# Kernel optimization log

Measured on AMD Instinct MI355X. Metric: run time of the kernel, lower is better.

## Reference

```python
import jax, jax.numpy as jnp
import numpy as np

N_NODES = 100000
N_EDGES = 1600000
HID = 32


def gcn_conv(x, W, b, src, dst, num_nodes):
    # PyG GCNConv: h = X W; out = D^{-1/2}(A+I)D^{-1/2} h + b
    # (self loops already appended to src/dst by caller)
    h = x @ W
    deg = jax.ops.segment_sum(jnp.ones_like(dst, dtype=h.dtype), dst,
                              num_segments=num_nodes)
    dinv = jnp.where(deg > 0, jax.lax.rsqrt(deg), 0.0)
    norm = dinv[src] * dinv[dst]                      # [E+N]
    msg = h[src] * norm[:, None]                      # gather + scale
    out = jax.ops.segment_sum(msg, dst, num_segments=num_nodes)  # scatter-add
    return out + b


def setup_inputs() -> dict:
    key = jax.random.key(0)
    ks = jax.random.split(key, 12)
    x = jax.random.normal(ks[0], (N_NODES, 2), dtype=jnp.float32)
    edge_index = jax.random.randint(ks[1], (2, N_EDGES), 0, N_NODES,
                                    dtype=jnp.int32)
    s = 0.2  # small init scale
    return {
        "x": x,
        "edge_index": edge_index,
        "fc1_W": jax.random.normal(ks[2], (2, HID), jnp.float32) * s,
        "fc1_b": jnp.zeros((HID,), jnp.float32),
        "c1_W": jax.random.normal(ks[3], (HID, HID), jnp.float32) * s,
        "c1_b": jnp.zeros((HID,), jnp.float32),
        "c2_W": jax.random.normal(ks[4], (HID, HID), jnp.float32) * s,
        "c2_b": jnp.zeros((HID,), jnp.float32),
        "c3_W": jax.random.normal(ks[5], (HID, HID), jnp.float32) * s,
        "c3_b": jnp.zeros((HID,), jnp.float32),
        "fc2_W": jax.random.normal(ks[6], (HID, HID), jnp.float32) * s,
        "fc2_b": jnp.zeros((HID,), jnp.float32),
        "fc3_W": jax.random.normal(ks[7], (HID, 1), jnp.float32) * s,
        "fc3_b": jnp.zeros((1,), jnp.float32),
    }


def reference(x, edge_index, fc1_W, fc1_b, c1_W, c1_b, c2_W, c2_b,
              c3_W, c3_b, fc2_W, fc2_b, fc3_W, fc3_b):
    num_nodes = x.shape[0]
    loop = jnp.arange(num_nodes, dtype=edge_index.dtype)
    src = jnp.concatenate([edge_index[0], loop])  # add self loops
    dst = jnp.concatenate([edge_index[1], loop])
    h = jax.nn.relu(x @ fc1_W + fc1_b)
    h = jax.nn.relu(gcn_conv(h, c1_W, c1_b, src, dst, num_nodes))
    h = jax.nn.relu(gcn_conv(h, c2_W, c2_b, src, dst, num_nodes))
    h = jax.nn.relu(gcn_conv(h, c3_W, c3_b, src, dst, num_nodes))
    h = jax.nn.relu(h @ fc2_W + fc2_b)
    return h @ fc3_W + fc3_b
```

## Files before the change

kernel.cpp:

```cpp
#include <hip/hip_runtime.h>
#include <hip/hip_fp16.h>

#define NN 100000
#define NE 1600000
#define HID 32
#define NBK 391
#define CAP 4608
#define CHUNK 8192

__device__ __forceinline__ float4 load_h4(const __half* p) {
    uint2 u = *(const uint2*)p;
    __half2 h0 = *(__half2*)&u.x;
    __half2 h1 = *(__half2*)&u.y;
    float2 a = __half22float2(h0);
    float2 b = __half22float2(h1);
    return make_float4(a.x, a.y, b.x, b.y);
}

__global__ __launch_bounds__(256) void partA_kernel(
        const int* __restrict__ src, const int* __restrict__ dst,
        int* __restrict__ bktcur, int* __restrict__ bedges) {
    __shared__ int cache[CHUNK];
    __shared__ int hist[NBK];
    __shared__ int lofs[NBK];
    int t = threadIdx.x;
    int base = blockIdx.x * CHUNK;
    for (int i = t; i < NBK; i += 256) hist[i] = 0;
    __syncthreads();
    for (int i = t; i < CHUNK; i += 256) {
        int e = base + i;
        if (e < NE) {
            int d = dst[e];
            cache[i] = d;
            atomicAdd(&hist[d >> 8], 1);
        }
    }
    __syncthreads();
    for (int i = t; i < NBK; i += 256)
        lofs[i] = hist[i] ? atomicAdd(&bktcur[i], hist[i]) : 0;
    __syncthreads();
    for (int i = t; i < CHUNK; i += 256) {
        int e = base + i;
        if (e < NE) {
            int d = cache[i];
            int s = src[e];
            int b = d >> 8;
            int rel = atomicAdd(&lofs[b], 1);
            if (rel < CAP) bedges[b * CAP + rel] = (s << 8) | (d & 255);
        }
    }
}

__global__ __launch_bounds__(256) void bucket_csr_kernel(
        const int* __restrict__ bedges, const int* __restrict__ bktcur,
        const float* __restrict__ x, float* __restrict__ dinv,
        int* __restrict__ srcidx, int* __restrict__ rbeg, int* __restrict__ rend,
        float4* __restrict__ xpack) {
    __shared__ int ldeg[256];
    __shared__ int lcur[256];
    __shared__ int wsum[256];
    int b = blockIdx.x, t = threadIdx.x;
    int ebeg = b * CAP;
    int cnt = min(bktcur[b], CAP);
    int n0 = b << 8;
    ldeg[t] = 0;
    __syncthreads();
    for (int e = t; e < cnt; e += 256)
        atomicAdd(&ldeg[bedges[ebeg + e] & 255], 1);
    __syncthreads();
    int a = ldeg[t];
    wsum[t] = a;
    __syncthreads();
    for (int off = 1; off < 256; off <<= 1) {
        int xv = (t >= off) ? wsum[t - off] : 0;
        __syncthreads();
        wsum[t] += xv;
        __syncthreads();
    }
    int excl = wsum[t] - a;
    lcur[t] = excl;
    int n = n0 + t;
    if (n < NN) {
        float dv = rsqrtf((float)(a + 1));
        rbeg[n] = ebeg + excl;
        rend[n] = ebeg + excl + a;
        dinv[n] = dv;
        float2 xv2 = *(const float2*)&x[2 * n];
        xpack[n] = make_float4(xv2.x, xv2.y, dv, 0.f);
    }
    __syncthreads();
    for (int e = t; e < cnt; e += 256) {
        int w = bedges[ebeg + e];
        int pos = atomicAdd(&lcur[w & 255], 1);
        srcidx[ebeg + pos] = (unsigned)w >> 8;
    }
}

__global__ __launch_bounds__(256) void conv1_kernel(
        const float4* __restrict__ xpack, const int* __restrict__ rbeg,
        const int* __restrict__ rend, const int* __restrict__ srcidx,
        const float* __restrict__ dinv, const float* __restrict__ W1,
        const float* __restrict__ b1, const float* __restrict__ W,
        const float* __restrict__ bias, __half* __restrict__ hs_out) {
    __shared__ float wl[HID * HID];
    __shared__ float agg[8][HID];
    int tid = threadIdx.x;
    int base8 = blockIdx.x * 8;
#pragma unroll
    for (int i = 0; i < 4; ++i) wl[tid + 256 * i] = W[tid + 256 * i];
    int wave = tid >> 6, lane = tid & 63;
    int g = lane >> 3;
    int l = lane & 7;
    float4 w0q = *(const float4*)&W1[l << 2];
    float4 w1q = *(const float4*)&W1[HID + (l << 2)];
    float4 bq  = *(const float4*)&b1[l << 2];
#pragma unroll
    for (int rep = 0; rep < 2; ++rep) {
        int ln = wave * 2 + rep;
        int n = base8 + ln;
        int beg = rbeg[n], end = rend[n];
        float4 acc0 = make_float4(0.f, 0.f, 0.f, 0.f);
        float4 acc1 = make_float4(0.f, 0.f, 0.f, 0.f);
        int e = beg + g;
        for (; e + 8 < end; e += 16) {
            float4 p0 = xpack[srcidx[e]];
            float4 p1 = xpack[srcidx[e + 8]];
            acc0.x += fmaxf(p0.x * w0q.x + p0.y * w1q.x + bq.x, 0.f) * p0.z;
            acc0.y += fmaxf(p0.x * w0q.y + p0.y * w1q.y + bq.y, 0.f) * p0.z;
            acc0.z += fmaxf(p0.x * w0q.z + p0.y * w1q.z + bq.z, 0.f) * p0.z;
            acc0.w += fmaxf(p0.x * w0q.w + p0.y * w1q.w + bq.w, 0.f) * p0.z;
            acc1.x += fmaxf(p1.x * w0q.x + p1.y * w1q.x + bq.x, 0.f) * p1.z;
            acc1.y += fmaxf(p1.x * w0q.y + p1.y * w1q.y + bq.y, 0.f) * p1.z;
            acc1.z += fmaxf(p1.x * w0q.z + p1.y * w1q.z + bq.z, 0.f) * p1.z;
            acc1.w += fmaxf(p1.x * w0q.w + p1.y * w1q.w + bq.w, 0.f) * p1.z;
        }
        if (e < end) {
            float4 p0 = xpack[srcidx[e]];
            acc0.x += fmaxf(p0.x * w0q.x + p0.y * w1q.x + bq.x, 0.f) * p0.z;
            acc0.y += fmaxf(p0.x * w0q.y + p0.y * w1q.y + bq.y, 0.f) * p0.z;
            acc0.z += fmaxf(p0.x * w0q.z + p0.y * w1q.z + bq.z, 0.f) * p0.z;
            acc0.w += fmaxf(p0.x * w0q.w + p0.y * w1q.w + bq.w, 0.f) * p0.z;
        }
        acc0.x += acc1.x; acc0.y += acc1.y; acc0.z += acc1.z; acc0.w += acc1.w;
#pragma unroll
        for (int m = 8; m < 64; m <<= 1) {
            acc0.x += __shfl_xor(acc0.x, m);
            acc0.y += __shfl_xor(acc0.y, m);
            acc0.z += __shfl_xor(acc0.z, m);
            acc0.w += __shfl_xor(acc0.w, m);
        }
        if (g == 0) {
            float4 ps = xpack[n];
            float dv = ps.z;
            float4 r;
            r.x = (acc0.x + fmaxf(ps.x * w0q.x + ps.y * w1q.x + bq.x, 0.f) * dv) * dv;
            r.y = (acc0.y + fmaxf(ps.x * w0q.y + ps.y * w1q.y + bq.y, 0.f) * dv) * dv;
            r.z = (acc0.z + fmaxf(ps.x * w0q.z + ps.y * w1q.z + bq.z, 0.f) * dv) * dv;
            r.w = (acc0.w + fmaxf(ps.x * w0q.w + ps.y * w1q.w + bq.w, 0.f) * dv) * dv;
            *(float4*)&agg[ln][l << 2] = r;
        }
    }
    __syncthreads();
    int ln = tid >> 5, j = tid & 31;
    int n = base8 + ln;
    float v = 0.f;
#pragma unroll
    for (int k = 0; k < HID; ++k) v += agg[ln][k] * wl[k * HID + j];
    v = fmaxf(v + bias[j], 0.f) * dinv[n];
    hs_out[(n << 5) + j] = __float2half(v);
}

template <bool OUTSCALE, bool FUSE23>
__global__ __launch_bounds__(256) void conv_fused_kernel(
        const __half* __restrict__ hs_in, const int* __restrict__ rbeg,
        const int* __restrict__ rend, const int* __restrict__ srcidx,
        const float* __restrict__ dinv, const float* __restrict__ W,
        const float* __restrict__ bias, const float* __restrict__ W2,
        const float* __restrict__ b2, const float* __restrict__ W3,
        const float* __restrict__ b3, void* __restrict__ hs_out_v) {
    __shared__ float wl[HID * HID];
    __shared__ float wl2[FUSE23 ? HID * HID : 1];
    __shared__ float agg[8][HID];
    int tid = threadIdx.x;
    int base8 = blockIdx.x * 8;
#pragma unroll
    for (int i = 0; i < 4; ++i) wl[tid + 256 * i] = W[tid + 256 * i];
    if (FUSE23) {
#pragma unroll
        for (int i = 0; i < 4; ++i) wl2[tid + 256 * i] = W2[tid + 256 * i];
    }
    int wave = tid >> 6, lane = tid & 63;
    int g = lane >> 3;
    int l = lane & 7;
#pragma unroll
    for (int rep = 0; rep < 2; ++rep) {
        int ln = wave * 2 + rep;
        int n = base8 + ln;
        int beg = rbeg[n], end = rend[n];
        float4 acc0 = make_float4(0.f, 0.f, 0.f, 0.f);
        float4 acc1 = make_float4(0.f, 0.f, 0.f, 0.f);
        int e = beg + g;
        for (; e + 8 < end; e += 16) {
            int s0 = srcidx[e];
            int s1 = srcidx[e + 8];
            float4 v0 = load_h4(&hs_in[(s0 << 5) + (l << 2)]);
            float4 v1 = load_h4(&hs_in[(s1 << 5) + (l << 2)]);
            acc0.x += v0.x; acc0.y += v0.y; acc0.z += v0.z; acc0.w += v0.w;
            acc1.x += v1.x; acc1.y += v1.y; acc1.z += v1.z; acc1.w += v1.w;
        }
        if (e < end) {
            int s0 = srcidx[e];
            float4 v0 = load_h4(&hs_in[(s0 << 5) + (l << 2)]);
            acc0.x += v0.x; acc0.y += v0.y; acc0.z += v0.z; acc0.w += v0.w;
        }
        acc0.x += acc1.x; acc0.y += acc1.y; acc0.z += acc1.z; acc0.w += acc1.w;
#pragma unroll
        for (int m = 8; m < 64; m <<= 1) {
            acc0.x += __shfl_xor(acc0.x, m);
            acc0.y += __shfl_xor(acc0.y, m);
            acc0.z += __shfl_xor(acc0.z, m);
            acc0.w += __shfl_xor(acc0.w, m);
        }
        if (g == 0) {
            float4 self = load_h4(&hs_in[(n << 5) + (l << 2)]);
            float dv = dinv[n];
            float4 r;
            r.x = (acc0.x + self.x) * dv;
            r.y = (acc0.y + self.y) * dv;
            r.z = (acc0.z + self.z) * dv;
            r.w = (acc0.w + self.w) * dv;
            *(float4*)&agg[ln][l << 2] = r;
        }
    }
    __syncthreads();
    int ln = tid >> 5, j = tid & 31;
    int n = base8 + ln;
    float v = 0.f;
#pragma unroll
    for (int k = 0; k < HID; ++k) v += agg[ln][k] * wl[k * HID + j];
    v = fmaxf(v + bias[j], 0.f);
    if (OUTSCALE) v *= dinv[n];
    if (!FUSE23) {
        ((__half*)hs_out_v)[(n << 5) + j] = __float2half(v);
    } else {
        __syncthreads();
        agg[ln][j] = v;
        __syncthreads();
        float v2 = 0.f;
#pragma unroll
        for (int k = 0; k < HID; ++k) v2 += agg[ln][k] * wl2[k * HID + j];
        v2 = fmaxf(v2 + b2[j], 0.f);
        float p = v2 * W3[j];
#pragma unroll
        for (int m = 16; m; m >>= 1) p += __shfl_xor(p, m);
        if (j == 0) ((float*)hs_out_v)[n] = p + b3[0];
    }
}

extern "C" void kernel_launch(void* const* d_in, const int* in_sizes, int n_in,
                              void* d_out, int out_size, void* d_ws, size_t ws_size,
                              hipStream_t stream) {
    const float* x     = (const float*)d_in[0];
    const int*   ei    = (const int*)d_in[1];
    const float* fc1_W = (const float*)d_in[2];
    const float* fc1_b = (const float*)d_in[3];
    const float* c1_W  = (const float*)d_in[4];
    const float* c1_b  = (const float*)d_in[5];
    const float* c2_W  = (const float*)d_in[6];
    const float* c2_b  = (const float*)d_in[7];
    const float* c3_W  = (const float*)d_in[8];
    const float* c3_b  = (const float*)d_in[9];
    const float* fc2_W = (const float*)d_in[10];
    const float* fc2_b = (const float*)d_in[11];
    const float* fc3_W = (const float*)d_in[12];
    const float* fc3_b = (const float*)d_in[13];

    const int* src = ei;
    const int* dst = ei + NE;

    float*  ws     = (float*)d_ws;
    float*  dinv   = ws;
    __half* hA     = (__half*)(ws + NN);
    __half* hB     = (__half*)(ws + NN + NN * HID);
    float4* xpack  = (float4*)(ws + NN + 2 * NN * HID);
    int*    srcidx = (int*)(xpack + NN);
    int*    rbeg   = srcidx + NBK * CAP;
    int*    rend   = rbeg + NN;
    int*    bktcur = rend + NN;
    int*    bedges = (int*)hB;

    float* out = (float*)d_out;

    const int B = 256;
    const int gNH = (NN * HID) / B;
    const int gPart = (NE + CHUNK - 1) / CHUNK;

    hipMemsetAsync(bktcur, 0, NBK * sizeof(int), stream);
    partA_kernel<<<gPart, B, 0, stream>>>(src, dst, bktcur, bedges);
    bucket_csr_kernel<<<NBK, B, 0, stream>>>(bedges, bktcur, x, dinv, srcidx, rbeg, rend, xpack);

    conv1_kernel<<<gNH, B, 0, stream>>>(xpack, rbeg, rend, srcidx, dinv,
                                        fc1_W, fc1_b, c1_W, c1_b, hA);
    conv_fused_kernel<true, false><<<gNH, B, 0, stream>>>(
        hA, rbeg, rend, srcidx, dinv, c2_W, c2_b, nullptr, nullptr, nullptr, nullptr, hB);
    conv_fused_kernel<false, true><<<gNH, B, 0, stream>>>(
        hB, rbeg, rend, srcidx, dinv, c3_W, c3_b, fc2_W, fc2_b, fc3_W, fc3_b, out);
}
```

Measured before the change: 181.6 us.

## Interleave two-node gathers, use per-wave weight copies, split fc2/fc3 kernel

```diff
diff --git a/kernel.cpp b/kernel.cpp
--- a/kernel.cpp
+++ b/kernel.cpp
@@ -15,6 +15,9 @@
     float2 a = __half22float2(h0);
     float2 b = __half22float2(h1);
     return make_float4(a.x, a.y, b.x, b.y);
+}
+__device__ __forceinline__ void acc4(float4& a, const float4& v) {
+    a.x += v.x; a.y += v.y; a.z += v.z; a.w += v.w;
 }
 
 __global__ __launch_bounds__(256) void partA_kernel(
@@ -99,162 +102,173 @@
 __global__ __launch_bounds__(256) void conv1_kernel(
         const float4* __restrict__ xpack, const int* __restrict__ rbeg,
         const int* __restrict__ rend, const int* __restrict__ srcidx,
-        const float* __restrict__ dinv, const float* __restrict__ W1,
-        const float* __restrict__ b1, const float* __restrict__ W,
-        const float* __restrict__ bias, __half* __restrict__ hs_out) {
-    __shared__ float wl[HID * HID];
+        const float* __restrict__ W1, const float* __restrict__ b1,
+        const float* __restrict__ W, const float* __restrict__ bias,
+        __half* __restrict__ hs_out) {
+    __shared__ float wl[4][HID * HID];
     __shared__ float agg[8][HID];
     int tid = threadIdx.x;
+    int wave = tid >> 6, lane = tid & 63;
     int base8 = blockIdx.x * 8;
-#pragma unroll
-    for (int i = 0; i < 4; ++i) wl[tid + 256 * i] = W[tid + 256 * i];
-    int wave = tid >> 6, lane = tid & 63;
+    for (int i = lane; i < HID * HID; i += 64) wl[wave][i] = W[i];
     int g = lane >> 3;
     int l = lane & 7;
     float4 w0q = *(const float4*)&W1[l << 2];
     float4 w1q = *(const float4*)&W1[HID + (l << 2)];
     float4 bq  = *(const float4*)&b1[l << 2];
-#pragma unroll
-    for (int rep = 0; rep < 2; ++rep) {
-        int ln = wave * 2 + rep;
-        int n = base8 + ln;
-        int beg = rbeg[n], end = rend[n];
-        float4 acc0 = make_float4(0.f, 0.f, 0.f, 0.f);
-        float4 acc1 = make_float4(0.f, 0.f, 0.f, 0.f);
-        int e = beg + g;
-        for (; e + 8 < end; e += 16) {
-            float4 p0 = xpack[srcidx[e]];
-            float4 p1 = xpack[srcidx[e + 8]];
-            acc0.x += fmaxf(p0.x * w0q.x + p0.y * w1q.x + bq.x, 0.f) * p0.z;
-            acc0.y += fmaxf(p0.x * w0q.y + p0.y * w1q.y + bq.y, 0.f) * p0.z;
-            acc0.z += fmaxf(p0.x * w0q.z + p0.y * w1q.z + bq.z, 0.f) * p0.z;
-            acc0.w += fmaxf(p0.x * w0q.w + p0.y * w1q.w + bq.w, 0.f) * p0.z;
-            acc1.x += fmaxf(p1.x * w0q.x + p1.y * w1q.x + bq.x, 0.f) * p1.z;
-            acc1.y += fmaxf(p1.x * w0q.y + p1.y * w1q.y + bq.y, 0.f) * p1.z;
-            acc1.z += fmaxf(p1.x * w0q.z + p1.y * w1q.z + bq.z, 0.f) * p1.z;
-            acc1.w += fmaxf(p1.x * w0q.w + p1.y * w1q.w + bq.w, 0.f) * p1.z;
-        }
-        if (e < end) {
-            float4 p0 = xpack[srcidx[e]];
-            acc0.x += fmaxf(p0.x * w0q.x + p0.y * w1q.x + bq.x, 0.f) * p0.z;
-            acc0.y += fmaxf(p0.x * w0q.y + p0.y * w1q.y + bq.y, 0.f) * p0.z;
-            acc0.z += fmaxf(p0.x * w0q.z + p0.y * w1q.z + bq.z, 0.f) * p0.z;
-            acc0.w += fmaxf(p0.x * w0q.w + p0.y * w1q.w + bq.w, 0.f) * p0.z;
-        }
-        acc0.x += acc1.x; acc0.y += acc1.y; acc0.z += acc1.z; acc0.w += acc1.w;
-#pragma unroll
-        for (int m = 8; m < 64; m <<= 1) {
-            acc0.x += __shfl_xor(acc0.x, m);
-            acc0.y += __shfl_xor(acc0.y, m);
-            acc0.z += __shfl_xor(acc0.z, m);
-            acc0.w += __shfl_xor(acc0.w, m);
-        }
-        if (g == 0) {
-            float4 ps = xpack[n];
-            float dv = ps.z;
-            float4 r;
-            r.x = (acc0.x + fmaxf(ps.x * w0q.x + ps.y * w1q.x + bq.x, 0.f) * dv) * dv;
-            r.y = (acc0.y + fmaxf(ps.x * w0q.y + ps.y * w1q.y + bq.y, 0.f) * dv) * dv;
-            r.z = (acc0.z + fmaxf(ps.x * w0q.z + ps.y * w1q.z + bq.z, 0.f) * dv) * dv;
-            r.w = (acc0.w + fmaxf(ps.x * w0q.w + ps.y * w1q.w + bq.w, 0.f) * dv) * dv;
-            *(float4*)&agg[ln][l << 2] = r;
-        }
-    }
-    __syncthreads();
+    int n0 = base8 + wave * 2, n1 = n0 + 1;
+    float4 ps0 = xpack[n0];
+    float4 ps1 = xpack[n1];
+    int p0 = rbeg[n0] + g, q0 = rend[n0];
+    int p1 = rbeg[n1] + g, q1 = rend[n1];
+    float4 A0 = make_float4(0.f, 0.f, 0.f, 0.f), B0 = A0, A1 = A0, B1 = A0;
+#define FC1ROW(dstacc, P)                                                      \
+    {                                                                          \
+        dstacc.x += fmaxf(P.x * w0q.x + P.y * w1q.x + bq.x, 0.f) * P.z;        \
+        dstacc.y += fmaxf(P.x * w0q.y + P.y * w1q.y + bq.y, 0.f) * P.z;        \
+        dstacc.z += fmaxf(P.x * w0q.z + P.y * w1q.z + bq.z, 0.f) * P.z;        \
+        dstacc.w += fmaxf(P.x * w0q.w + P.y * w1q.w + bq.w, 0.f) * P.z;        \
+    }
+    for (; p0 + 8 < q0 && p1 + 8 < q1; p0 += 16, p1 += 16) {
+        float4 v00 = xpack[srcidx[p0]];
+        float4 v01 = xpack[srcidx[p0 + 8]];
+        float4 v10 = xpack[srcidx[p1]];
+        float4 v11 = xpack[srcidx[p1 + 8]];
+        FC1ROW(A0, v00); FC1ROW(B0, v01); FC1ROW(A1, v10); FC1ROW(B1, v11);
+    }
+    for (; p0 + 8 < q0; p0 += 16) {
+        float4 v00 = xpack[srcidx[p0]];
+        float4 v01 = xpack[srcidx[p0 + 8]];
+        FC1ROW(A0, v00); FC1ROW(B0, v01);
+    }
+    for (; p0 < q0; p0 += 8) { float4 v = xpack[srcidx[p0]]; FC1ROW(A0, v); }
+    for (; p1 + 8 < q1; p1 += 16) {
+        float4 v10 = xpack[srcidx[p1]];
+        float4 v11 = xpack[srcidx[p1 + 8]];
+        FC1ROW(A1, v10); FC1ROW(B1, v11);
+    }
+    for (; p1 < q1; p1 += 8) { float4 v = xpack[srcidx[p1]]; FC1ROW(A1, v); }
+    acc4(A0, B0); acc4(A1, B1);
+#pragma unroll
+    for (int m = 8; m < 64; m <<= 1) {
+        A0.x += __shfl_xor(A0.x, m); A1.x += __shfl_xor(A1.x, m);
+        A0.y += __shfl_xor(A0.y, m); A1.y += __shfl_xor(A1.y, m);
+        A0.z += __shfl_xor(A0.z, m); A1.z += __shfl_xor(A1.z, m);
+        A0.w += __shfl_xor(A0.w, m); A1.w += __shfl_xor(A1.w, m);
+    }
+    if (g == 0) {
+        float4 r0 = A0, r1 = A1;
+        FC1ROW(r0, ps0);
+        FC1ROW(r1, ps1);
+        r0.x *= ps0.z; r0.y *= ps0.z; r0.z *= ps0.z; r0.w *= ps0.z;
+        r1.x *= ps1.z; r1.y *= ps1.z; r1.z *= ps1.z; r1.w *= ps1.z;
+        *(float4*)&agg[wave * 2][l << 2] = r0;
+        *(float4*)&agg[wave * 2 + 1][l << 2] = r1;
+    }
+#undef FC1ROW
     int ln = tid >> 5, j = tid & 31;
     int n = base8 + ln;
+    float dv = ((lane >> 5) & 1) ? ps1.z : ps0.z;
     float v = 0.f;
 #pragma unroll
-    for (int k = 0; k < HID; ++k) v += agg[ln][k] * wl[k * HID + j];
-    v = fmaxf(v + bias[j], 0.f) * dinv[n];
+    for (int k = 0; k < HID; ++k) v += agg[ln][k] * wl[wave][k * HID + j];
+    v = fmaxf(v + bias[j], 0.f) * dv;
     hs_out[(n << 5) + j] = __float2half(v);
 }
 
-template <bool OUTSCALE, bool FUSE23>
+template <bool OUTSCALE>
 __global__ __launch_bounds__(256) void conv_fused_kernel(
         const __half* __restrict__ hs_in, const int* __restrict__ rbeg,
         const int* __restrict__ rend, const int* __restrict__ srcidx,
         const float* __restrict__ dinv, const float* __restrict__ W,
-        const float* __restrict__ bias, const float* __restrict__ W2,
-        const float* __restrict__ b2, const float* __restrict__ W3,
-        const float* __restrict__ b3, void* __restrict__ hs_out_v) {
-    __shared__ float wl[HID * HID];
-    __shared__ float wl2[FUSE23 ? HID * HID : 1];
+        const float* __restrict__ bias, __half* __restrict__ hs_out) {
+    __shared__ float wl[4][HID * HID];
     __shared__ float agg[8][HID];
     int tid = threadIdx.x;
+    int wave = tid >> 6, lane = tid & 63;
     int base8 = blockIdx.x * 8;
-#pragma unroll
-    for (int i = 0; i < 4; ++i) wl[tid + 256 * i] = W[tid + 256 * i];
-    if (FUSE23) {
-#pragma unroll
-        for (int i = 0; i < 4; ++i) wl2[tid + 256 * i] = W2[tid + 256 * i];
-    }
-    int wave = tid >> 6, lane = tid & 63;
+    for (int i = lane; i < HID * HID; i += 64) wl[wave][i] = W[i];
     int g = lane >> 3;
     int l = lane & 7;
-#pragma unroll
-    for (int rep = 0; rep < 2; ++rep) {
-        int ln = wave * 2 + rep;
-        int n = base8 + ln;
-        int beg = rbeg[n], end = rend[n];
-        float4 acc0 = make_float4(0.f, 0.f, 0.f, 0.f);
-        float4 acc1 = make_float4(0.f, 0.f, 0.f, 0.f);
-        int e = beg + g;
-        for (; e + 8 < end; e += 16) {
-            int s0 = srcidx[e];
-            int s1 = srcidx[e + 8];
-            float4 v0 = load_h4(&hs_in[(s0 << 5) + (l << 2)]);
-            float4 v1 = load_h4(&hs_in[(s1 << 5) + (l << 2)]);
-            acc0.x += v0.x; acc0.y += v0.y; acc0.z += v0.z; acc0.w += v0.w;
-            acc1.x += v1.x; acc1.y += v1.y; acc1.z += v1.z; acc1.w += v1.w;
-        }
-        if (e < end) {
-            int s0 = srcidx[e];
-            float4 v0 = load_h4(&hs_in[(s0 << 5) + (l << 2)]);
-            acc0.x += v0.x; acc0.y += v0.y; acc0.z += v0.z; acc0.w += v0.w;
-        }
-        acc0.x += acc1.x; acc0.y += acc1.y; acc0.z += acc1.z; acc0.w += acc1.w;
-#pragma unroll
-        for (int m = 8; m < 64; m <<= 1) {
-            acc0.x += __shfl_xor(acc0.x, m);
-            acc0.y += __shfl_xor(acc0.y, m);
-            acc0.z += __shfl_xor(acc0.z, m);
-            acc0.w += __shfl_xor(acc0.w, m);
-        }
-        if (g == 0) {
-            float4 self = load_h4(&hs_in[(n << 5) + (l << 2)]);
-            float dv = dinv[n];
-            float4 r;
-            r.x = (acc0.x + self.x) * dv;
-            r.y = (acc0.y + self.y) * dv;
-            r.z = (acc0.z + self.z) * dv;
-            r.w = (acc0.w + self.w) * dv;
-            *(float4*)&agg[ln][l << 2] = r;
-        }
-    }
-    __syncthreads();
+    int n0 = base8 + wave * 2, n1 = n0 + 1;
+    float4 self0 = load_h4(&hs_in[(n0 << 5) + (l << 2)]);
+    float4 self1 = load_h4(&hs_in[(n1 << 5) + (l << 2)]);
+    float dv0 = dinv[n0], dv1 = dinv[n1];
+    int p0 = rbeg[n0] + g, q0 = rend[n0];
+    int p1 = rbeg[n1] + g, q1 = rend[n1];
+    float4 A0 = make_float4(0.f, 0.f, 0.f, 0.f), B0 = A0, A1 = A0, B1 = A0;
+    for (; p0 + 8 < q0 && p1 + 8 < q1; p0 += 16, p1 += 16) {
+        int s00 = srcidx[p0], s01 = srcidx[p0 + 8];
+        int s10 = srcidx[p1], s11 = srcidx[p1 + 8];
+        float4 v00 = load_h4(&hs_in[(s00 << 5) + (l << 2)]);
+        float4 v01 = load_h4(&hs_in[(s01 << 5) + (l << 2)]);
+        float4 v10 = load_h4(&hs_in[(s10 << 5) + (l << 2)]);
+        float4 v11 = load_h4(&hs_in[(s11 << 5) + (l << 2)]);
+        acc4(A0, v00); acc4(B0, v01); acc4(A1, v10); acc4(B1, v11);
+    }
+    for (; p0 + 8 < q0; p0 += 16) {
+        int s00 = srcidx[p0], s01 = srcidx[p0 + 8];
+        float4 v00 = load_h4(&hs_in[(s00 << 5) + (l << 2)]);
+        float4 v01 = load_h4(&hs_in[(s01 << 5) + (l << 2)]);
+        acc4(A0, v00); acc4(B0, v01);
+    }
+    for (; p0 < q0; p0 += 8) acc4(A0, load_h4(&hs_in[(srcidx[p0] << 5) + (l << 2)]));
+    for (; p1 + 8 < q1; p1 += 16) {
+        int s10 = srcidx[p1], s11 = srcidx[p1 + 8];
+        float4 v10 = load_h4(&hs_in[(s10 << 5) + (l << 2)]);
+        float4 v11 = load_h4(&hs_in[(s11 << 5) + (l << 2)]);
+        acc4(A1, v10); acc4(B1, v11);
+    }
+    for (; p1 < q1; p1 += 8) acc4(A1, load_h4(&hs_in[(srcidx[p1] << 5) + (l << 2)]));
+    acc4(A0, B0); acc4(A1, B1);
+#pragma unroll
+    for (int m = 8; m < 64; m <<= 1) {
+        A0.x += __shfl_xor(A0.x, m); A1.x += __shfl_xor(A1.x, m);
+        A0.y += __shfl_xor(A0.y, m); A1.y += __shfl_xor(A1.y, m);
+        A0.z += __shfl_xor(A0.z, m); A1.z += __shfl_xor(A1.z, m);
+        A0.w += __shfl_xor(A0.w, m); A1.w += __shfl_xor(A1.w, m);
+    }
+    if (g == 0) {
+        float4 r0, r1;
+        r0.x = (A0.x + self0.x) * dv0; r0.y = (A0.y + self0.y) * dv0;
+        r0.z = (A0.z + self0.z) * dv0; r0.w = (A0.w + self0.w) * dv0;
+        r1.x = (A1.x + self1.x) * dv1; r1.y = (A1.y + self1.y) * dv1;
+        r1.z = (A1.z + self1.z) * dv1; r1.w = (A1.w + self1.w) * dv1;
+        *(float4*)&agg[wave * 2][l << 2] = r0;
+        *(float4*)&agg[wave * 2 + 1][l << 2] = r1;
+    }
     int ln = tid >> 5, j = tid & 31;
     int n = base8 + ln;
+    float dv = ((lane >> 5) & 1) ? dv1 : dv0;
     float v = 0.f;
 #pragma unroll
-    for (int k = 0; k < HID; ++k) v += agg[ln][k] * wl[k * HID + j];
+    for (int k = 0; k < HID; ++k) v += agg[ln][k] * wl[wave][k * HID + j];
     v = fmaxf(v + bias[j], 0.f);
-    if (OUTSCALE) v *= dinv[n];
-    if (!FUSE23) {
-        ((__half*)hs_out_v)[(n << 5) + j] = __float2half(v);
-    } else {
-        __syncthreads();
-        agg[ln][j] = v;
-        __syncthreads();
-        float v2 = 0.f;
-#pragma unroll
-        for (int k = 0; k < HID; ++k) v2 += agg[ln][k] * wl2[k * HID + j];
-        v2 = fmaxf(v2 + b2[j], 0.f);
-        float p = v2 * W3[j];
-#pragma unroll
-        for (int m = 16; m; m >>= 1) p += __shfl_xor(p, m);
-        if (j == 0) ((float*)hs_out_v)[n] = p + b3[0];
-    }
+    if (OUTSCALE) v *= dv;
+    hs_out[(n << 5) + j] = __float2half(v);
+}
+
+__global__ __launch_bounds__(256) void fc23_kernel(
+        const __half* __restrict__ h, const float* __restrict__ W2,
+        const float* __restrict__ b2, const float* __restrict__ W3,
+        const float* __restrict__ b3, float* __restrict__ out) {
+    __shared__ float wl[HID * HID];
+    __shared__ float hsl[256];
+    int tid = threadIdx.x;
+    int base = blockIdx.x * 256;
+#pragma unroll
+    for (int i = 0; i < 4; ++i) wl[tid + 256 * i] = W2[tid + 256 * i];
+    hsl[tid] = __half2float(h[base + tid]);
+    __syncthreads();
+    int ln = tid >> 5, j = tid & 31;
+    float v = 0.f;
+#pragma unroll
+    for (int k = 0; k < HID; ++k) v += hsl[ln * HID + k] * wl[k * HID + j];
+    v = fmaxf(v + b2[j], 0.f);
+    float p = v * W3[j];
+#pragma unroll
+    for (int m = 16; m; m >>= 1) p += __shfl_xor(p, m);
+    if (j == 0) out[(base >> 5) + ln] = p + b3[0];
 }
 
 extern "C" void kernel_launch(void* const* d_in, const int* in_sizes, int n_in,
@@ -299,10 +313,11 @@
     partA_kernel<<<gPart, B, 0, stream>>>(src, dst, bktcur, bedges);
     bucket_csr_kernel<<<NBK, B, 0, stream>>>(bedges, bktcur, x, dinv, srcidx, rbeg, rend, xpack);
 
-    conv1_kernel<<<gNH, B, 0, stream>>>(xpack, rbeg, rend, srcidx, dinv,
+    conv1_kernel<<<gNH, B, 0, stream>>>(xpack, rbeg, rend, srcidx,
                                         fc1_W, fc1_b, c1_W, c1_b, hA);
-    conv_fused_kernel<true, false><<<gNH, B, 0, stream>>>(
-        hA, rbeg, rend, srcidx, dinv, c2_W, c2_b, nullptr, nullptr, nullptr, nullptr, hB);
-    conv_fused_kernel<false, true><<<gNH, B, 0, stream>>>(
-        hB, rbeg, rend, srcidx, dinv, c3_W, c3_b, fc2_W, fc2_b, fc3_W, fc3_b, out);
-}
+    conv_fused_kernel<true><<<gNH, B, 0, stream>>>(
+        hA, rbeg, rend, srcidx, dinv, c2_W, c2_b, hB);
+    conv_fused_kernel<false><<<gNH, B, 0, stream>>>(
+        hB, rbeg, rend, srcidx, dinv, c3_W, c3_b, hA);
+    fc23_kernel<<<gNH, B, 0, stream>>>(hA, fc2_W, fc2_b, fc3_W, fc3_b, out);
+}
```

Result: slower. 207.0 us (+14.0%).
